# Optimization experiments

Hardware: AMD Instinct MI355X
Metric: run time of the kernel (lower is better)

The kernel has to match this reference:

```python
import jax, jax.numpy as jnp
import numpy as np

NUM_EXPERTS = 8
TOP_K = 2
IN_DIM = 2048
BOT_DIM = 512
BATCH, SEQ = 4, 2048


def setup_inputs() -> dict:
    key = jax.random.key(0)
    ks = jax.random.split(key, 8)
    scale_d = 1.0 / np.sqrt(IN_DIM)
    scale_b = 1.0 / np.sqrt(BOT_DIM)
    return {
        "hidden_states": jax.random.normal(ks[0], (BATCH, SEQ, IN_DIM), jnp.float32),
        # gate: nn.Linear(in_dim, num_experts, bias=False) -> weight [E, D]
        "gate_w": jax.random.normal(ks[1], (NUM_EXPERTS, IN_DIM), jnp.float32) * scale_d,
        # routed experts: down weight [E, B, D], down bias [E, B], up weight [E, D, B], up bias [E, D]
        # (original inits up weights/biases to zero; use small random so grads are non-trivial)
        "wd": jax.random.normal(ks[2], (NUM_EXPERTS, BOT_DIM, IN_DIM), jnp.float32) * scale_d,
        "bd": jnp.zeros((NUM_EXPERTS, BOT_DIM), jnp.float32),
        "wu": jax.random.normal(ks[3], (NUM_EXPERTS, IN_DIM, BOT_DIM), jnp.float32) * scale_b * 0.02,
        "bu": jnp.zeros((NUM_EXPERTS, IN_DIM), jnp.float32),
        # one shared Bottleneck_adapter
        "ws_d": jax.random.normal(ks[4], (BOT_DIM, IN_DIM), jnp.float32) * scale_d,
        "bs_d": jnp.zeros((BOT_DIM,), jnp.float32),
        "ws_u": jax.random.normal(ks[5], (IN_DIM, BOT_DIM), jnp.float32) * scale_b * 0.02,
        "bs_u": jnp.zeros((IN_DIM,), jnp.float32),
    }


def _gelu(x):
    # torch.nn.GELU() default = exact erf form
    return jax.nn.gelu(x, approximate=False)


def reference(hidden_states, gate_w, wd, bd, wu, bu, ws_d, bs_d, ws_u, bs_u):
    B, S, D = hidden_states.shape
    x = hidden_states.reshape(-1, D)                      # [T, D]
    T = x.shape[0]

    # --- top-k softmax routing (softmax in fp32, renormalize top-k weights) ---
    logits = x @ gate_w.T                                 # [T, E]
    probs = jax.nn.softmax(logits.astype(jnp.float32), axis=-1)
    rw, sel = jax.lax.top_k(probs, TOP_K)                 # [T, K]
    rw = rw / rw.sum(axis=-1, keepdims=True)
    rw = rw.astype(x.dtype)

    # dense combine weights [T, E]: zero for unselected experts == skipping them
    combine = jnp.zeros((T, NUM_EXPERTS), x.dtype).at[
        jnp.arange(T)[:, None], sel
    ].add(rw)

    # --- routed experts: bottleneck FFN per expert, combined by routing weight ---
    down = jnp.einsum('td,ebd->teb', x, wd) + bd[None]    # [T, E, Bn]
    h = _gelu(down) * combine[:, :, None]                 # weight before up-proj (linear)
    expert_out = jnp.einsum('teb,edb->td', h, wu) + combine @ bu  # [T, D]

    # --- shared expert (applied to original hidden states) ---
    shared = _gelu(x @ ws_d.T + bs_d) @ ws_u.T + bs_u

    out = (expert_out + shared).reshape(B, S, D)
    return out
```

## Files before the change

kernel.cpp:

```cpp
#include <hip/hip_runtime.h>
#include <hip/hip_bf16.h>

typedef __bf16 bf16_t;
typedef __bf16 bf16x8 __attribute__((ext_vector_type(8)));
typedef float f32x4 __attribute__((ext_vector_type(4)));

#define T_TOK 8192
#define D_IN  2048
#define D_BOT 512
#define MAXTILES 192
#define MAXDTILES 200

union U4B8 { uint4 u; bf16x8 b; };
__device__ __forceinline__ bf16x8 as_bf16x8(uint4 u) { U4B8 x; x.u = u; return x.b; }
__device__ __forceinline__ uint4 as_uint4(bf16x8 b) { U4B8 x; x.b = b; return x.u; }

typedef const __attribute__((address_space(1))) void gas_void;
typedef __attribute__((address_space(3))) void las_void;
__device__ __forceinline__ void async16(const void* g, void* l) {
    __builtin_amdgcn_global_load_lds((gas_void*)g, (las_void*)l, 16, 0, 0);
}

__device__ __forceinline__ uint4 ld_cvt8(const float* __restrict__ p) {
    f32x4 a0 = ((const f32x4*)p)[0];
    f32x4 a1 = ((const f32x4*)p)[1];
    bf16x8 v;
    v[0] = (bf16_t)a0[0]; v[1] = (bf16_t)a0[1]; v[2] = (bf16_t)a0[2]; v[3] = (bf16_t)a0[3];
    v[4] = (bf16_t)a1[0]; v[5] = (bf16_t)a1[1]; v[6] = (bf16_t)a1[2]; v[7] = (bf16_t)a1[3];
    return as_uint4(v);
}

__device__ __forceinline__ float gelu_f(float v) {
    return 0.5f * v * (1.0f + erff(v * 0.7071067811865476f));
}

__global__ __launch_bounds__(256) void cvt_kernel(const float* __restrict__ src,
                                                  bf16_t* __restrict__ dst, int n8) {
    const int i = blockIdx.x * 256 + threadIdx.x;
    if (i < n8) ((uint4*)dst)[i] = ld_cvt8(src + (size_t)i * 8);
}

__global__ __launch_bounds__(256) void cvt4_kernel(const float* __restrict__ wd,
                                                   const float* __restrict__ wsd,
                                                   const float* __restrict__ wu,
                                                   const float* __restrict__ wsu,
                                                   bf16_t* __restrict__ WallD,
                                                   bf16_t* __restrict__ WallU) {
    const int i = blockIdx.x * 256 + threadIdx.x;
    const int N0 = 4096 * 2048 / 8;
    const int N1 = N0 + 512 * 2048 / 8;
    const int N2 = N1 + 8 * 2048 * 512 / 8;
    const int N3 = N2 + 2048 * 512 / 8;
    if (i < N0)      ((uint4*)WallD)[i] = ld_cvt8(wd + (size_t)i * 8);
    else if (i < N1) ((uint4*)WallD)[i] = ld_cvt8(wsd + (size_t)(i - N0) * 8);
    else if (i < N2) ((uint4*)WallU)[i - N1] = ld_cvt8(wu + (size_t)(i - N1) * 8);
    else if (i < N3) ((uint4*)WallU)[i - N1] = ld_cvt8(wsu + (size_t)(i - N2) * 8);
}

__global__ __launch_bounds__(256) void gate_kernel(const float* __restrict__ x,
                                                   const float* __restrict__ gw,
                                                   float* __restrict__ combine,
                                                   int* __restrict__ sel,
                                                   bf16_t* __restrict__ Xbf) {
    const int wave = threadIdx.x >> 6, lane = threadIdx.x & 63;
    const int t = blockIdx.x * 4 + wave;
    const float* xrow = x + (size_t)t * D_IN;
    f32x4 xa[4][2];
#pragma unroll
    for (int c = 0; c < 4; ++c) {
        const float* p = xrow + c * 512 + lane * 8;
        xa[c][0] = ((const f32x4*)p)[0];
        xa[c][1] = ((const f32x4*)p)[1];
    }
#pragma unroll
    for (int c = 0; c < 4; ++c) {
        bf16x8 v;
#pragma unroll
        for (int j = 0; j < 4; ++j) { v[j] = (bf16_t)xa[c][0][j]; v[4 + j] = (bf16_t)xa[c][1][j]; }
        *(uint4*)(Xbf + (size_t)t * D_IN + c * 512 + lane * 8) = as_uint4(v);
    }
    float p[8];
#pragma unroll
    for (int e = 0; e < 8; ++e) {
        const float* gr = gw + e * D_IN;
        float s = 0.f;
#pragma unroll
        for (int c = 0; c < 4; ++c) {
            const float* q = gr + c * 512 + lane * 8;
            f32x4 g0 = ((const f32x4*)q)[0], g1 = ((const f32x4*)q)[1];
#pragma unroll
            for (int j = 0; j < 4; ++j) s += xa[c][0][j] * g0[j] + xa[c][1][j] * g1[j];
        }
#pragma unroll
        for (int off = 32; off > 0; off >>= 1) s += __shfl_xor(s, off, 64);
        p[e] = s;
    }
    float m = p[0];
#pragma unroll
    for (int e = 1; e < 8; ++e) m = fmaxf(m, p[e]);
    float sum = 0.f;
#pragma unroll
    for (int e = 0; e < 8; ++e) { p[e] = expf(p[e] - m); sum += p[e]; }
    const float inv = 1.0f / sum;
#pragma unroll
    for (int e = 0; e < 8; ++e) p[e] *= inv;
    int i0 = 0;
#pragma unroll
    for (int e = 1; e < 8; ++e) if (p[e] > p[i0]) i0 = e;
    int i1 = -1;
#pragma unroll
    for (int e = 0; e < 8; ++e) { if (e == i0) continue; if (i1 < 0 || p[e] > p[i1]) i1 = e; }
    const float rs = 1.0f / (p[i0] + p[i1]);
    if (lane < 8)
        combine[t * 8 + lane] = (lane == i0) ? p[i0] * rs : (lane == i1) ? p[i1] * rs : 0.0f;
    if (lane == 0) sel[t] = i0 | (i1 << 4);
}

__global__ __launch_bounds__(256) void build_kernel(const int* __restrict__ sel,
                                                    int* __restrict__ meta,
                                                    int* __restrict__ tokE,
                                                    int* __restrict__ tokP) {
    __shared__ unsigned short cAll[8][256];
    __shared__ unsigned short cP[64][256];
    const int tid = threadIdx.x;
#pragma unroll
    for (int e = 0; e < 8; ++e) cAll[e][tid] = 0;
#pragma unroll
    for (int p = 0; p < 64; ++p) cP[p][tid] = 0;
    __syncthreads();
    int sl[32];
#pragma unroll
    for (int j = 0; j < 32; ++j) sl[j] = sel[tid * 32 + j];
#pragma unroll
    for (int j = 0; j < 32; ++j) {
        const int e0 = sl[j] & 15, e1 = sl[j] >> 4;
        cAll[e0][tid]++; cAll[e1][tid]++; cP[e0 * 8 + e1][tid]++;
    }
    __syncthreads();
    if (tid < 8) {
        unsigned short* arr = cAll[tid];
        int run = 0;
        for (int i = 0; i < 256; ++i) { int v = arr[i]; arr[i] = (unsigned short)run; run += v; }
        meta[tid] = run;
    } else if (tid >= 64 && tid < 128) {
        unsigned short* arr = cP[tid - 64];
        int run = 0;
        for (int i = 0; i < 256; ++i) { int v = arr[i]; arr[i] = (unsigned short)run; run += v; }
        meta[64 + (tid - 64)] = run;
    }
    __syncthreads();
    if (tid == 0) {
        int nt = 0;
        for (int p = 0; p < 64; ++p) {
            const int c = meta[64 + p];
            for (int s = 0; s < c; s += 64) { meta[128 + nt] = p; meta[320 + nt] = s; ++nt; }
        }
        meta[8] = nt;
        int nd = 0;
        for (int e = 0; e < 9; ++e) {
            const int c = (e < 8) ? meta[e] : T_TOK;
            for (int s = 0; s < c; s += 128) { meta[512 + nd] = e; meta[768 + nd] = s; ++nd; }
        }
        meta[9] = nd;
    }
#pragma unroll
    for (int j = 0; j < 32; ++j) {
        const int t = tid * 32 + j, e0 = sl[j] & 15, e1 = sl[j] >> 4;
        const int p0 = cAll[e0][tid]++;  tokE[e0 * 8192 + p0] = t;
        const int p1 = cAll[e1][tid]++;  tokE[e1 * 8192 + p1] = t | 65536;
        const int q  = cP[e0 * 8 + e1][tid]++;  tokP[(e0 * 8 + e1) * 8192 + q] = t;
    }
}

__global__ __launch_bounds__(256) void down_kernel(const bf16_t* __restrict__ Xbf,
                                                   const bf16_t* __restrict__ Wall,
                                                   const float* __restrict__ Bd,
                                                   const float* __restrict__ Bsd,
                                                   const float* __restrict__ combine,
                                                   const int* __restrict__ meta,
                                                   const int* __restrict__ tokE,
                                                   bf16_t* __restrict__ Ht) {
    __shared__ uint4 As4[128 * 8];
    __shared__ uint4 Bs4[64 * 8];
    const int orig = blockIdx.x;
    const int swz = (orig & 7) * 200 + (orig >> 3);
    const int yt = swz >> 3;
    const int tile_n = (swz & 7) * 64;
    if (yt >= meta[9]) return;
    const int e = meta[512 + yt];
    const int m0 = meta[768 + yt];
    const int count = (e < 8) ? meta[e] : T_TOK;
    const int tid = threadIdx.x, lane = tid & 63, wv = tid >> 6;
    const int wm = wv >> 1, wn = wv & 1;
    const int gB = (lane & 7) ^ ((lane >> 3) & 7);

    const bf16_t* aAddr[4];
    const bf16_t* bAddr[2];
#pragma unroll
    for (int j = 0; j < 4; ++j) {
        const int rr = (wv * 4 + j) * 8 + (lane >> 3);
        int gi = m0 + rr; if (gi > count - 1) gi = count - 1;
        const int t = (e < 8) ? (tokE[e * 8192 + gi] & 0xFFFF) : gi;
        aAddr[j] = Xbf + (size_t)t * D_IN + gB * 8;
    }
#pragma unroll
    for (int j = 0; j < 2; ++j) {
        const int rr = (wv * 2 + j) * 8 + (lane >> 3);
        bAddr[j] = Wall + (size_t)(e * 512 + tile_n + rr) * D_IN + gB * 8;
    }

    f32x4 acc[4][2];
#pragma unroll
    for (int i = 0; i < 4; ++i)
#pragma unroll
        for (int j = 0; j < 2; ++j) acc[i][j] = (f32x4){0.f, 0.f, 0.f, 0.f};

    for (int kt = 0; kt < D_IN / 64; ++kt) {
        const int k0 = kt * 64;
#pragma unroll
        for (int j = 0; j < 4; ++j)
            async16(aAddr[j] + k0, &As4[(wv * 4 + j) * 64]);
#pragma unroll
        for (int j = 0; j < 2; ++j)
            async16(bAddr[j] + k0, &Bs4[(wv * 2 + j) * 64]);
        __syncthreads();
#pragma unroll
        for (int ks = 0; ks < 2; ++ks) {
            bf16x8 af[4], bfr[2];
#pragma unroll
            for (int i = 0; i < 4; ++i) {
                const int ar = wm * 64 + i * 16 + (lane & 15);
                af[i] = as_bf16x8(As4[ar * 8 + ((ks * 4 + (lane >> 4)) ^ (lane & 7))]);
            }
#pragma unroll
            for (int i = 0; i < 2; ++i) {
                const int br = wn * 32 + i * 16 + (lane & 15);
                bfr[i] = as_bf16x8(Bs4[br * 8 + ((ks * 4 + (lane >> 4)) ^ (lane & 7))]);
            }
#pragma unroll
            for (int mi = 0; mi < 4; ++mi)
#pragma unroll
                for (int nj = 0; nj < 2; ++nj)
                    acc[mi][nj] = __builtin_amdgcn_mfma_f32_16x16x32_bf16(
                        af[mi], bfr[nj], acc[mi][nj], 0, 0, 0);
        }
        __syncthreads();
    }

#pragma unroll
    for (int nj = 0; nj < 2; ++nj) {
        const int nn = tile_n + wn * 32 + nj * 16 + (lane & 15);
        const float bias = (e < 8) ? Bd[e * 512 + nn] : Bsd[nn];
#pragma unroll
        for (int mi = 0; mi < 4; ++mi) {
            const int g0 = m0 + wm * 64 + mi * 16 + ((lane >> 4) << 2);
#pragma unroll
            for (int r = 0; r < 4; ++r) {
                const int gi = g0 + r;
                if (gi >= count) continue;
                if (e < 8) {
                    const int entry = tokE[e * 8192 + gi];
                    const int t = entry & 0xFFFF, rank = entry >> 16;
                    const float v = gelu_f(acc[mi][nj][r] + bias) * combine[t * 8 + e];
                    Ht[(size_t)t * 1536 + rank * 512 + nn] = (bf16_t)v;
                } else {
                    Ht[(size_t)gi * 1536 + 1024 + nn] = (bf16_t)gelu_f(acc[mi][nj][r] + bias);
                }
            }
        }
    }
}

__global__ __launch_bounds__(256) void up_kernel(const bf16_t* __restrict__ Ht,
                                                 const bf16_t* __restrict__ Wup,
                                                 const float* __restrict__ Bu,
                                                 const float* __restrict__ Bsu,
                                                 const float* __restrict__ combine,
                                                 const int* __restrict__ meta,
                                                 const int* __restrict__ tokP,
                                                 float* __restrict__ Out) {
    __shared__ uint4 As4[64 * 8];
    __shared__ uint4 Bs4[128 * 8];
    const int orig = blockIdx.x;
    const int swz = (orig & 7) * 384 + (orig >> 3);
    const int yt = swz >> 4;
    const int tile_n = (swz & 15) * 128;
    if (yt >= meta[8]) return;
    const int p = meta[128 + yt], s = meta[320 + yt];
    const int e0 = p >> 3, e1 = p & 7;
    const int cntP = meta[64 + p];
    const int tid = threadIdx.x, lane = tid & 63, wv = tid >> 6;
    const int wm = wv >> 1, wn = wv & 1;
    const int gB = (lane & 7) ^ ((lane >> 3) & 7);

    const bf16_t* aAddr[2];
#pragma unroll
    for (int j = 0; j < 2; ++j) {
        const int rr = (wv * 2 + j) * 8 + (lane >> 3);
        int gi = s + rr; if (gi > cntP - 1) gi = cntP - 1;
        const int t = tokP[p * 8192 + gi];
        aAddr[j] = Ht + (size_t)t * 1536 + gB * 8;
    }
    size_t bRow[4];
#pragma unroll
    for (int j = 0; j < 4; ++j) {
        const int rr = (wv * 4 + j) * 8 + (lane >> 3);
        bRow[j] = (size_t)(tile_n + rr) * D_BOT + gB * 8;
    }

    f32x4 acc[2][4];
#pragma unroll
    for (int i = 0; i < 2; ++i)
#pragma unroll
        for (int j = 0; j < 4; ++j) acc[i][j] = (f32x4){0.f, 0.f, 0.f, 0.f};

    for (int kt = 0; kt < 24; ++kt) {
        const int seg = kt >> 3;
        const int slot = (seg == 0) ? e0 : (seg == 1) ? e1 : 8;
        const bf16_t* wbase = Wup + (size_t)slot * (D_IN * D_BOT) + (kt & 7) * 64;
#pragma unroll
        for (int j = 0; j < 2; ++j)
            async16(aAddr[j] + kt * 64, &As4[(wv * 2 + j) * 64]);
#pragma unroll
        for (int j = 0; j < 4; ++j)
            async16(wbase + bRow[j], &Bs4[(wv * 4 + j) * 64]);
        __syncthreads();
#pragma unroll
        for (int ks = 0; ks < 2; ++ks) {
            bf16x8 af[2], bfr[4];
#pragma unroll
            for (int i = 0; i < 2; ++i) {
                const int ar = wm * 32 + i * 16 + (lane & 15);
                af[i] = as_bf16x8(As4[ar * 8 + ((ks * 4 + (lane >> 4)) ^ (lane & 7))]);
            }
#pragma unroll
            for (int i = 0; i < 4; ++i) {
                const int br = wn * 64 + i * 16 + (lane & 15);
                bfr[i] = as_bf16x8(Bs4[br * 8 + ((ks * 4 + (lane >> 4)) ^ (lane & 7))]);
            }
#pragma unroll
            for (int mi = 0; mi < 2; ++mi)
#pragma unroll
                for (int nj = 0; nj < 4; ++nj)
                    acc[mi][nj] = __builtin_amdgcn_mfma_f32_16x16x32_bf16(
                        af[mi], bfr[nj], acc[mi][nj], 0, 0, 0);
        }
        __syncthreads();
    }

#pragma unroll
    for (int nj = 0; nj < 4; ++nj) {
        const int d = tile_n + wn * 64 + nj * 16 + (lane & 15);
        const float bu0 = Bu[e0 * D_IN + d], bu1 = Bu[e1 * D_IN + d], bs = Bsu[d];
#pragma unroll
        for (int mi = 0; mi < 2; ++mi) {
            const int r0 = wm * 32 + mi * 16 + ((lane >> 4) << 2);
#pragma unroll
            for (int r = 0; r < 4; ++r) {
                const int gi = s + r0 + r;
                if (gi >= cntP) continue;
                const int t = tokP[p * 8192 + gi];
                const float c0 = combine[t * 8 + e0], c1 = combine[t * 8 + e1];
                Out[(size_t)t * D_IN + d] = acc[mi][nj][r] + c0 * bu0 + c1 * bu1 + bs;
            }
        }
    }
}

extern "C" void kernel_launch(void* const* d_in, const int* in_sizes, int n_in,
                              void* d_out, int out_size, void* d_ws, size_t ws_size,
                              hipStream_t stream) {
    const float* x   = (const float*)d_in[0];
    const float* gw  = (const float*)d_in[1];
    const float* wd  = (const float*)d_in[2];
    const float* bd  = (const float*)d_in[3];
    const float* wu  = (const float*)d_in[4];
    const float* bu  = (const float*)d_in[5];
    const float* wsd = (const float*)d_in[6];
    const float* bsd = (const float*)d_in[7];
    const float* wsu = (const float*)d_in[8];
    const float* bsu = (const float*)d_in[9];
    float* out = (float*)d_out;

    char* ws = (char*)d_ws;
    float* combine = (float*)(ws + 0);
    int*   meta    = (int*)(ws + 262144);
    int*   sel     = (int*)(ws + 266240);
    int*   tokE    = (int*)(ws + 299008);
    int*   tokP    = (int*)(ws + 561152);
    bf16_t* Xbf    = (bf16_t*)(ws + 2658304);
    bf16_t* Ht     = (bf16_t*)(ws + 36212736ull);
    bf16_t* WallD  = (bf16_t*)(ws + 61378560ull);
    const size_t NEED_SEP = 61378560ull + 2ull * 18874368ull;
    const bool separate = (ws_size >= NEED_SEP);
    bf16_t* WallU  = separate ? (bf16_t*)(ws + 61378560ull + 18874368ull) : WallD;

    gate_kernel<<<T_TOK / 4, 256, 0, stream>>>(x, gw, combine, sel, Xbf);
    build_kernel<<<1, 256, 0, stream>>>(sel, meta, tokE, tokP);

    if (separate) {
        cvt4_kernel<<<9216, 256, 0, stream>>>(wd, wsd, wu, wsu, WallD, WallU);
        down_kernel<<<MAXDTILES * 8, 256, 0, stream>>>(Xbf, WallD, bd, bsd, combine, meta, tokE, Ht);
        up_kernel<<<MAXTILES * 16, 256, 0, stream>>>(Ht, WallU, bu, bsu, combine, meta, tokP, out);
    } else {
        cvt_kernel<<<(4096 * D_IN / 8) / 256, 256, 0, stream>>>(wd, WallD, 4096 * D_IN / 8);
        cvt_kernel<<<(512 * D_IN / 8) / 256, 256, 0, stream>>>(wsd, WallD + (size_t)4096 * D_IN, 512 * D_IN / 8);
        down_kernel<<<MAXDTILES * 8, 256, 0, stream>>>(Xbf, WallD, bd, bsd, combine, meta, tokE, Ht);
        cvt_kernel<<<(8 * D_IN * D_BOT / 8) / 256, 256, 0, stream>>>(wu, WallD, 8 * D_IN * D_BOT / 8);
        cvt_kernel<<<(D_IN * D_BOT / 8) / 256, 256, 0, stream>>>(wsu, WallD + (size_t)8 * D_IN * D_BOT, D_IN * D_BOT / 8);
        up_kernel<<<MAXTILES * 16, 256, 0, stream>>>(Ht, WallD, bu, bsu, combine, meta, tokP, out);
    }
}
```

Before: 450.9 us.

## Double-buffer LDS tiles in down and up GEMM kernels with async prefetch

Both grouped GEMM kernels now keep two LDS buffers and issue global-to-LDS async loads two k-steps ahead, waiting with explicit vmcnt counters before each compute step. The aim is to hide global memory latency behind MFMA work, where previously every k-step loaded and then stalled on a full sync. This doubles LDS use per block, which may lower occupancy, and it depends on manual waitcnt values matching the count of outstanding loads (6 per stage).

```diff
diff --git a/kernel.cpp b/kernel.cpp
--- a/kernel.cpp
+++ b/kernel.cpp
@@ -180,8 +180,8 @@
                                                    const int* __restrict__ meta,
                                                    const int* __restrict__ tokE,
                                                    bf16_t* __restrict__ Ht) {
-    __shared__ uint4 As4[128 * 8];
-    __shared__ uint4 Bs4[64 * 8];
+    __shared__ uint4 As4[2][128 * 8];
+    __shared__ uint4 Bs4[2][64 * 8];
     const int orig = blockIdx.x;
     const int swz = (orig & 7) * 200 + (orig >> 3);
     const int yt = swz >> 3;
@@ -215,27 +215,28 @@
 #pragma unroll
         for (int j = 0; j < 2; ++j) acc[i][j] = (f32x4){0.f, 0.f, 0.f, 0.f};
 
-    for (int kt = 0; kt < D_IN / 64; ++kt) {
+    auto stage = [&](int b, int kt) {
         const int k0 = kt * 64;
 #pragma unroll
         for (int j = 0; j < 4; ++j)
-            async16(aAddr[j] + k0, &As4[(wv * 4 + j) * 64]);
+            async16(aAddr[j] + k0, &As4[b][(wv * 4 + j) * 64]);
 #pragma unroll
         for (int j = 0; j < 2; ++j)
-            async16(bAddr[j] + k0, &Bs4[(wv * 2 + j) * 64]);
-        __syncthreads();
+            async16(bAddr[j] + k0, &Bs4[b][(wv * 2 + j) * 64]);
+    };
+    auto compute = [&](int b) {
 #pragma unroll
         for (int ks = 0; ks < 2; ++ks) {
             bf16x8 af[4], bfr[2];
 #pragma unroll
             for (int i = 0; i < 4; ++i) {
                 const int ar = wm * 64 + i * 16 + (lane & 15);
-                af[i] = as_bf16x8(As4[ar * 8 + ((ks * 4 + (lane >> 4)) ^ (lane & 7))]);
+                af[i] = as_bf16x8(As4[b][ar * 8 + ((ks * 4 + (lane >> 4)) ^ (lane & 7))]);
             }
 #pragma unroll
             for (int i = 0; i < 2; ++i) {
                 const int br = wn * 32 + i * 16 + (lane & 15);
-                bfr[i] = as_bf16x8(Bs4[br * 8 + ((ks * 4 + (lane >> 4)) ^ (lane & 7))]);
+                bfr[i] = as_bf16x8(Bs4[b][br * 8 + ((ks * 4 + (lane >> 4)) ^ (lane & 7))]);
             }
 #pragma unroll
             for (int mi = 0; mi < 4; ++mi)
@@ -244,7 +245,18 @@
                     acc[mi][nj] = __builtin_amdgcn_mfma_f32_16x16x32_bf16(
                         af[mi], bfr[nj], acc[mi][nj], 0, 0, 0);
         }
-        __syncthreads();
+    };
+
+    const int NT = D_IN / 64;
+    stage(0, 0);
+    stage(1, 1);
+    for (int kt = 0; kt < NT; ++kt) {
+        if (kt == NT - 1) asm volatile("s_waitcnt vmcnt(0)" ::: "memory");
+        else              asm volatile("s_waitcnt vmcnt(6)" ::: "memory");
+        __builtin_amdgcn_s_barrier();
+        compute(kt & 1);
+        __builtin_amdgcn_s_barrier();
+        if (kt + 2 < NT) stage(kt & 1, kt + 2);
     }
 
 #pragma unroll
@@ -279,8 +291,8 @@
                                                  const int* __restrict__ meta,
                                                  const int* __restrict__ tokP,
                                                  float* __restrict__ Out) {
-    __shared__ uint4 As4[64 * 8];
-    __shared__ uint4 Bs4[128 * 8];
+    __shared__ uint4 As4[2][64 * 8];
+    __shared__ uint4 Bs4[2][128 * 8];
     const int orig = blockIdx.x;
     const int swz = (orig & 7) * 384 + (orig >> 3);
     const int yt = swz >> 4;
@@ -314,29 +326,30 @@
 #pragma unroll
         for (int j = 0; j < 4; ++j) acc[i][j] = (f32x4){0.f, 0.f, 0.f, 0.f};
 
-    for (int kt = 0; kt < 24; ++kt) {
+    auto stage = [&](int b, int kt) {
         const int seg = kt >> 3;
         const int slot = (seg == 0) ? e0 : (seg == 1) ? e1 : 8;
         const bf16_t* wbase = Wup + (size_t)slot * (D_IN * D_BOT) + (kt & 7) * 64;
 #pragma unroll
         for (int j = 0; j < 2; ++j)
-            async16(aAddr[j] + kt * 64, &As4[(wv * 2 + j) * 64]);
+            async16(aAddr[j] + kt * 64, &As4[b][(wv * 2 + j) * 64]);
 #pragma unroll
         for (int j = 0; j < 4; ++j)
-            async16(wbase + bRow[j], &Bs4[(wv * 4 + j) * 64]);
-        __syncthreads();
+            async16(wbase + bRow[j], &Bs4[b][(wv * 4 + j) * 64]);
+    };
+    auto compute = [&](int b) {
 #pragma unroll
         for (int ks = 0; ks < 2; ++ks) {
             bf16x8 af[2], bfr[4];
 #pragma unroll
             for (int i = 0; i < 2; ++i) {
                 const int ar = wm * 32 + i * 16 + (lane & 15);
-                af[i] = as_bf16x8(As4[ar * 8 + ((ks * 4 + (lane >> 4)) ^ (lane & 7))]);
+                af[i] = as_bf16x8(As4[b][ar * 8 + ((ks * 4 + (lane >> 4)) ^ (lane & 7))]);
             }
 #pragma unroll
             for (int i = 0; i < 4; ++i) {
                 const int br = wn * 64 + i * 16 + (lane & 15);
-                bfr[i] = as_bf16x8(Bs4[br * 8 + ((ks * 4 + (lane >> 4)) ^ (lane & 7))]);
+                bfr[i] = as_bf16x8(Bs4[b][br * 8 + ((ks * 4 + (lane >> 4)) ^ (lane & 7))]);
             }
 #pragma unroll
             for (int mi = 0; mi < 2; ++mi)
@@ -345,7 +358,18 @@
                     acc[mi][nj] = __builtin_amdgcn_mfma_f32_16x16x32_bf16(
                         af[mi], bfr[nj], acc[mi][nj], 0, 0, 0);
         }
-        __syncthreads();
+    };
+
+    const int NT = 24;
+    stage(0, 0);
+    stage(1, 1);
+    for (int kt = 0; kt < NT; ++kt) {
+        if (kt == NT - 1) asm volatile("s_waitcnt vmcnt(0)" ::: "memory");
+        else              asm volatile("s_waitcnt vmcnt(6)" ::: "memory");
+        __builtin_amdgcn_s_barrier();
+        compute(kt & 1);
+        __builtin_amdgcn_s_barrier();
+        if (kt + 2 < NT) stage(kt & 1, kt + 2);
     }
 
 #pragma unroll
```

After: 496.1 us. +10.0%, slower.

## Merge gate with weight conversion and run GEMM kernels with 512-thread blocks

Applied to the files above, without the earlier changes.

Combines the gating/routing kernel and the fp32-to-bf16 weight conversion into one launch so the two independent jobs share the GPU and one launch is saved. The down and up GEMM kernels move to 8 waves per block, each wave holding a smaller accumulator tile (2x2 MFMA fragments) and issuing fewer async loads. This aims to raise occupancy and latency hiding, but more waves contend on the per-k-step barrier, and the block tile shapes appear unchanged.

```diff
diff --git a/kernel.cpp b/kernel.cpp
--- a/kernel.cpp
+++ b/kernel.cpp
@@ -40,13 +40,87 @@
     if (i < n8) ((uint4*)dst)[i] = ld_cvt8(src + (size_t)i * 8);
 }
 
-__global__ __launch_bounds__(256) void cvt4_kernel(const float* __restrict__ wd,
-                                                   const float* __restrict__ wsd,
-                                                   const float* __restrict__ wu,
-                                                   const float* __restrict__ wsu,
-                                                   bf16_t* __restrict__ WallD,
-                                                   bf16_t* __restrict__ WallU) {
-    const int i = blockIdx.x * 256 + threadIdx.x;
+__device__ __forceinline__ void gate_body(int bid,
+                                          const float* __restrict__ x,
+                                          const float* __restrict__ gw,
+                                          float* __restrict__ combine,
+                                          int* __restrict__ sel,
+                                          bf16_t* __restrict__ Xbf) {
+    const int wave = threadIdx.x >> 6, lane = threadIdx.x & 63;
+    const int t = bid * 4 + wave;
+    const float* xrow = x + (size_t)t * D_IN;
+    f32x4 xa[4][2];
+#pragma unroll
+    for (int c = 0; c < 4; ++c) {
+        const float* p = xrow + c * 512 + lane * 8;
+        xa[c][0] = ((const f32x4*)p)[0];
+        xa[c][1] = ((const f32x4*)p)[1];
+    }
+#pragma unroll
+    for (int c = 0; c < 4; ++c) {
+        bf16x8 v;
+#pragma unroll
+        for (int j = 0; j < 4; ++j) { v[j] = (bf16_t)xa[c][0][j]; v[4 + j] = (bf16_t)xa[c][1][j]; }
+        *(uint4*)(Xbf + (size_t)t * D_IN + c * 512 + lane * 8) = as_uint4(v);
+    }
+    float p[8];
+#pragma unroll
+    for (int e = 0; e < 8; ++e) {
+        const float* gr = gw + e * D_IN;
+        float s = 0.f;
+#pragma unroll
+        for (int c = 0; c < 4; ++c) {
+            const float* q = gr + c * 512 + lane * 8;
+            f32x4 g0 = ((const f32x4*)q)[0], g1 = ((const f32x4*)q)[1];
+#pragma unroll
+            for (int j = 0; j < 4; ++j) s += xa[c][0][j] * g0[j] + xa[c][1][j] * g1[j];
+        }
+#pragma unroll
+        for (int off = 32; off > 0; off >>= 1) s += __shfl_xor(s, off, 64);
+        p[e] = s;
+    }
+    float m = p[0];
+#pragma unroll
+    for (int e = 1; e < 8; ++e) m = fmaxf(m, p[e]);
+    float sum = 0.f;
+#pragma unroll
+    for (int e = 0; e < 8; ++e) { p[e] = expf(p[e] - m); sum += p[e]; }
+    const float inv = 1.0f / sum;
+#pragma unroll
+    for (int e = 0; e < 8; ++e) p[e] *= inv;
+    int i0 = 0;
+#pragma unroll
+    for (int e = 1; e < 8; ++e) if (p[e] > p[i0]) i0 = e;
+    int i1 = -1;
+#pragma unroll
+    for (int e = 0; e < 8; ++e) { if (e == i0) continue; if (i1 < 0 || p[e] > p[i1]) i1 = e; }
+    const float rs = 1.0f / (p[i0] + p[i1]);
+    if (lane < 8)
+        combine[t * 8 + lane] = (lane == i0) ? p[i0] * rs : (lane == i1) ? p[i1] * rs : 0.0f;
+    if (lane == 0) sel[t] = i0 | (i1 << 4);
+}
+
+__global__ __launch_bounds__(256) void gate_kernel(const float* __restrict__ x,
+                                                   const float* __restrict__ gw,
+                                                   float* __restrict__ combine,
+                                                   int* __restrict__ sel,
+                                                   bf16_t* __restrict__ Xbf) {
+    gate_body(blockIdx.x, x, gw, combine, sel, Xbf);
+}
+
+__global__ __launch_bounds__(256) void gate_cvt_kernel(const float* __restrict__ x,
+                                                       const float* __restrict__ gw,
+                                                       float* __restrict__ combine,
+                                                       int* __restrict__ sel,
+                                                       bf16_t* __restrict__ Xbf,
+                                                       const float* __restrict__ wd,
+                                                       const float* __restrict__ wsd,
+                                                       const float* __restrict__ wu,
+                                                       const float* __restrict__ wsu,
+                                                       bf16_t* __restrict__ WallD,
+                                                       bf16_t* __restrict__ WallU) {
+    if (blockIdx.x < 2048) { gate_body(blockIdx.x, x, gw, combine, sel, Xbf); return; }
+    const int i = (blockIdx.x - 2048) * 256 + threadIdx.x;
     const int N0 = 4096 * 2048 / 8;
     const int N1 = N0 + 512 * 2048 / 8;
     const int N2 = N1 + 8 * 2048 * 512 / 8;
@@ -55,65 +129,6 @@
     else if (i < N1) ((uint4*)WallD)[i] = ld_cvt8(wsd + (size_t)(i - N0) * 8);
     else if (i < N2) ((uint4*)WallU)[i - N1] = ld_cvt8(wu + (size_t)(i - N1) * 8);
     else if (i < N3) ((uint4*)WallU)[i - N1] = ld_cvt8(wsu + (size_t)(i - N2) * 8);
-}
-
-__global__ __launch_bounds__(256) void gate_kernel(const float* __restrict__ x,
-                                                   const float* __restrict__ gw,
-                                                   float* __restrict__ combine,
-                                                   int* __restrict__ sel,
-                                                   bf16_t* __restrict__ Xbf) {
-    const int wave = threadIdx.x >> 6, lane = threadIdx.x & 63;
-    const int t = blockIdx.x * 4 + wave;
-    const float* xrow = x + (size_t)t * D_IN;
-    f32x4 xa[4][2];
-#pragma unroll
-    for (int c = 0; c < 4; ++c) {
-        const float* p = xrow + c * 512 + lane * 8;
-        xa[c][0] = ((const f32x4*)p)[0];
-        xa[c][1] = ((const f32x4*)p)[1];
-    }
-#pragma unroll
-    for (int c = 0; c < 4; ++c) {
-        bf16x8 v;
-#pragma unroll
-        for (int j = 0; j < 4; ++j) { v[j] = (bf16_t)xa[c][0][j]; v[4 + j] = (bf16_t)xa[c][1][j]; }
-        *(uint4*)(Xbf + (size_t)t * D_IN + c * 512 + lane * 8) = as_uint4(v);
-    }
-    float p[8];
-#pragma unroll
-    for (int e = 0; e < 8; ++e) {
-        const float* gr = gw + e * D_IN;
-        float s = 0.f;
-#pragma unroll
-        for (int c = 0; c < 4; ++c) {
-            const float* q = gr + c * 512 + lane * 8;
-            f32x4 g0 = ((const f32x4*)q)[0], g1 = ((const f32x4*)q)[1];
-#pragma unroll
-            for (int j = 0; j < 4; ++j) s += xa[c][0][j] * g0[j] + xa[c][1][j] * g1[j];
-        }
-#pragma unroll
-        for (int off = 32; off > 0; off >>= 1) s += __shfl_xor(s, off, 64);
-        p[e] = s;
-    }
-    float m = p[0];
-#pragma unroll
-    for (int e = 1; e < 8; ++e) m = fmaxf(m, p[e]);
-    float sum = 0.f;
-#pragma unroll
-    for (int e = 0; e < 8; ++e) { p[e] = expf(p[e] - m); sum += p[e]; }
-    const float inv = 1.0f / sum;
-#pragma unroll
-    for (int e = 0; e < 8; ++e) p[e] *= inv;
-    int i0 = 0;
-#pragma unroll
-    for (int e = 1; e < 8; ++e) if (p[e] > p[i0]) i0 = e;
-    int i1 = -1;
-#pragma unroll
-    for (int e = 0; e < 8; ++e) { if (e == i0) continue; if (i1 < 0 || p[e] > p[i1]) i1 = e; }
-    const float rs = 1.0f / (p[i0] + p[i1]);
-    if (lane < 8)
-        combine[t * 8 + lane] = (lane == i0) ? p[i0] * rs : (lane == i1) ? p[i1] * rs : 0.0f;
-    if (lane == 0) sel[t] = i0 | (i1 << 4);
 }
 
 __global__ __launch_bounds__(256) void build_kernel(const int* __restrict__ sel,
@@ -172,7 +187,7 @@
     }
 }
 
-__global__ __launch_bounds__(256) void down_kernel(const bf16_t* __restrict__ Xbf,
+__global__ __launch_bounds__(512) void down_kernel(const bf16_t* __restrict__ Xbf,
                                                    const bf16_t* __restrict__ Wall,
                                                    const float* __restrict__ Bd,
                                                    const float* __restrict__ Bsd,
@@ -194,42 +209,39 @@
     const int wm = wv >> 1, wn = wv & 1;
     const int gB = (lane & 7) ^ ((lane >> 3) & 7);
 
-    const bf16_t* aAddr[4];
-    const bf16_t* bAddr[2];
-#pragma unroll
-    for (int j = 0; j < 4; ++j) {
-        const int rr = (wv * 4 + j) * 8 + (lane >> 3);
+    const bf16_t* aAddr[2];
+#pragma unroll
+    for (int j = 0; j < 2; ++j) {
+        const int rr = (wv * 2 + j) * 8 + (lane >> 3);
         int gi = m0 + rr; if (gi > count - 1) gi = count - 1;
         const int t = (e < 8) ? (tokE[e * 8192 + gi] & 0xFFFF) : gi;
         aAddr[j] = Xbf + (size_t)t * D_IN + gB * 8;
     }
-#pragma unroll
-    for (int j = 0; j < 2; ++j) {
-        const int rr = (wv * 2 + j) * 8 + (lane >> 3);
-        bAddr[j] = Wall + (size_t)(e * 512 + tile_n + rr) * D_IN + gB * 8;
-    }
-
-    f32x4 acc[4][2];
-#pragma unroll
-    for (int i = 0; i < 4; ++i)
+    const bf16_t* bAddr;
+    {
+        const int rr = wv * 8 + (lane >> 3);
+        bAddr = Wall + (size_t)(e * 512 + tile_n + rr) * D_IN + gB * 8;
+    }
+
+    f32x4 acc[2][2];
+#pragma unroll
+    for (int i = 0; i < 2; ++i)
 #pragma unroll
         for (int j = 0; j < 2; ++j) acc[i][j] = (f32x4){0.f, 0.f, 0.f, 0.f};
 
     for (int kt = 0; kt < D_IN / 64; ++kt) {
         const int k0 = kt * 64;
 #pragma unroll
-        for (int j = 0; j < 4; ++j)
-            async16(aAddr[j] + k0, &As4[(wv * 4 + j) * 64]);
-#pragma unroll
         for (int j = 0; j < 2; ++j)
-            async16(bAddr[j] + k0, &Bs4[(wv * 2 + j) * 64]);
+            async16(aAddr[j] + k0, &As4[(wv * 2 + j) * 64]);
+        async16(bAddr + k0, &Bs4[wv * 64]);
         __syncthreads();
 #pragma unroll
         for (int ks = 0; ks < 2; ++ks) {
-            bf16x8 af[4], bfr[2];
-#pragma unroll
-            for (int i = 0; i < 4; ++i) {
-                const int ar = wm * 64 + i * 16 + (lane & 15);
+            bf16x8 af[2], bfr[2];
+#pragma unroll
+            for (int i = 0; i < 2; ++i) {
+                const int ar = wm * 32 + i * 16 + (lane & 15);
                 af[i] = as_bf16x8(As4[ar * 8 + ((ks * 4 + (lane >> 4)) ^ (lane & 7))]);
             }
 #pragma unroll
@@ -238,7 +250,7 @@
                 bfr[i] = as_bf16x8(Bs4[br * 8 + ((ks * 4 + (lane >> 4)) ^ (lane & 7))]);
             }
 #pragma unroll
-            for (int mi = 0; mi < 4; ++mi)
+            for (int mi = 0; mi < 2; ++mi)
 #pragma unroll
                 for (int nj = 0; nj < 2; ++nj)
                     acc[mi][nj] = __builtin_amdgcn_mfma_f32_16x16x32_bf16(
@@ -252,8 +264,8 @@
         const int nn = tile_n + wn * 32 + nj * 16 + (lane & 15);
         const float bias = (e < 8) ? Bd[e * 512 + nn] : Bsd[nn];
 #pragma unroll
-        for (int mi = 0; mi < 4; ++mi) {
-            const int g0 = m0 + wm * 64 + mi * 16 + ((lane >> 4) << 2);
+        for (int mi = 0; mi < 2; ++mi) {
+            const int g0 = m0 + wm * 32 + mi * 16 + ((lane >> 4) << 2);
 #pragma unroll
             for (int r = 0; r < 4; ++r) {
                 const int gi = g0 + r;
@@ -271,7 +283,7 @@
     }
 }
 
-__global__ __launch_bounds__(256) void up_kernel(const bf16_t* __restrict__ Ht,
+__global__ __launch_bounds__(512) void up_kernel(const bf16_t* __restrict__ Ht,
                                                  const bf16_t* __restrict__ Wup,
                                                  const float* __restrict__ Bu,
                                                  const float* __restrict__ Bsu,
@@ -290,58 +302,55 @@
     const int e0 = p >> 3, e1 = p & 7;
     const int cntP = meta[64 + p];
     const int tid = threadIdx.x, lane = tid & 63, wv = tid >> 6;
-    const int wm = wv >> 1, wn = wv & 1;
+    const int wm = wv >> 2, wn = wv & 3;
     const int gB = (lane & 7) ^ ((lane >> 3) & 7);
 
-    const bf16_t* aAddr[2];
+    const bf16_t* aAddr;
+    {
+        const int rr = wv * 8 + (lane >> 3);
+        int gi = s + rr; if (gi > cntP - 1) gi = cntP - 1;
+        const int t = tokP[p * 8192 + gi];
+        aAddr = Ht + (size_t)t * 1536 + gB * 8;
+    }
+    size_t bRow[2];
 #pragma unroll
     for (int j = 0; j < 2; ++j) {
         const int rr = (wv * 2 + j) * 8 + (lane >> 3);
-        int gi = s + rr; if (gi > cntP - 1) gi = cntP - 1;
-        const int t = tokP[p * 8192 + gi];
-        aAddr[j] = Ht + (size_t)t * 1536 + gB * 8;
-    }
-    size_t bRow[4];
-#pragma unroll
-    for (int j = 0; j < 4; ++j) {
-        const int rr = (wv * 4 + j) * 8 + (lane >> 3);
         bRow[j] = (size_t)(tile_n + rr) * D_BOT + gB * 8;
     }
 
-    f32x4 acc[2][4];
+    f32x4 acc[2][2];
 #pragma unroll
     for (int i = 0; i < 2; ++i)
 #pragma unroll
-        for (int j = 0; j < 4; ++j) acc[i][j] = (f32x4){0.f, 0.f, 0.f, 0.f};
+        for (int j = 0; j < 2; ++j) acc[i][j] = (f32x4){0.f, 0.f, 0.f, 0.f};
 
     for (int kt = 0; kt < 24; ++kt) {
         const int seg = kt >> 3;
         const int slot = (seg == 0) ? e0 : (seg == 1) ? e1 : 8;
         const bf16_t* wbase = Wup + (size_t)slot * (D_IN * D_BOT) + (kt & 7) * 64;
+        async16(aAddr + kt * 64, &As4[wv * 64]);
 #pragma unroll
         for (int j = 0; j < 2; ++j)
-            async16(aAddr[j] + kt * 64, &As4[(wv * 2 + j) * 64]);
-#pragma unroll
-        for (int j = 0; j < 4; ++j)
-            async16(wbase + bRow[j], &Bs4[(wv * 4 + j) * 64]);
+            async16(wbase + bRow[j], &Bs4[(wv * 2 + j) * 64]);
         __syncthreads();
 #pragma unroll
         for (int ks = 0; ks < 2; ++ks) {
-            bf16x8 af[2], bfr[4];
+            bf16x8 af[2], bfr[2];
 #pragma unroll
             for (int i = 0; i < 2; ++i) {
                 const int ar = wm * 32 + i * 16 + (lane & 15);
                 af[i] = as_bf16x8(As4[ar * 8 + ((ks * 4 + (lane >> 4)) ^ (lane & 7))]);
             }
 #pragma unroll
-            for (int i = 0; i < 4; ++i) {
-                const int br = wn * 64 + i * 16 + (lane & 15);
+            for (int i = 0; i < 2; ++i) {
+                const int br = wn * 32 + i * 16 + (lane & 15);
                 bfr[i] = as_bf16x8(Bs4[br * 8 + ((ks * 4 + (lane >> 4)) ^ (lane & 7))]);
             }
 #pragma unroll
             for (int mi = 0; mi < 2; ++mi)
 #pragma unroll
-                for (int nj = 0; nj < 4; ++nj)
+                for (int nj = 0; nj < 2; ++nj)
                     acc[mi][nj] = __builtin_amdgcn_mfma_f32_16x16x32_bf16(
                         af[mi], bfr[nj], acc[mi][nj], 0, 0, 0);
         }
@@ -349,8 +358,8 @@
     }
 
 #pragma unroll
-    for (int nj = 0; nj < 4; ++nj) {
-        const int d = tile_n + wn * 64 + nj * 16 + (lane & 15);
+    for (int nj = 0; nj < 2; ++nj) {
+        const int d = tile_n + wn * 32 + nj * 16 + (lane & 15);
         const float bu0 = Bu[e0 * D_IN + d], bu1 = Bu[e1 * D_IN + d], bs = Bsu[d];
 #pragma unroll
         for (int mi = 0; mi < 2; ++mi) {
@@ -395,19 +404,20 @@
     const bool separate = (ws_size >= NEED_SEP);
     bf16_t* WallU  = separate ? (bf16_t*)(ws + 61378560ull + 18874368ull) : WallD;
 
-    gate_kernel<<<T_TOK / 4, 256, 0, stream>>>(x, gw, combine, sel, Xbf);
-    build_kernel<<<1, 256, 0, stream>>>(sel, meta, tokE, tokP);
-
     if (separate) {
-        cvt4_kernel<<<9216, 256, 0, stream>>>(wd, wsd, wu, wsu, WallD, WallU);
-        down_kernel<<<MAXDTILES * 8, 256, 0, stream>>>(Xbf, WallD, bd, bsd, combine, meta, tokE, Ht);
-        up_kernel<<<MAXTILES * 16, 256, 0, stream>>>(Ht, WallU, bu, bsu, combine, meta, tokP, out);
+        gate_cvt_kernel<<<2048 + 9216, 256, 0, stream>>>(x, gw, combine, sel, Xbf,
+                                                         wd, wsd, wu, wsu, WallD, WallU);
+        build_kernel<<<1, 256, 0, stream>>>(sel, meta, tokE, tokP);
+        down_kernel<<<MAXDTILES * 8, 512, 0, stream>>>(Xbf, WallD, bd, bsd, combine, meta, tokE, Ht);
+        up_kernel<<<MAXTILES * 16, 512, 0, stream>>>(Ht, WallU, bu, bsu, combine, meta, tokP, out);
     } else {
+        gate_kernel<<<T_TOK / 4, 256, 0, stream>>>(x, gw, combine, sel, Xbf);
+        build_kernel<<<1, 256, 0, stream>>>(sel, meta, tokE, tokP);
         cvt_kernel<<<(4096 * D_IN / 8) / 256, 256, 0, stream>>>(wd, WallD, 4096 * D_IN / 8);
         cvt_kernel<<<(512 * D_IN / 8) / 256, 256, 0, stream>>>(wsd, WallD + (size_t)4096 * D_IN, 512 * D_IN / 8);
-        down_kernel<<<MAXDTILES * 8, 256, 0, stream>>>(Xbf, WallD, bd, bsd, combine, meta, tokE, Ht);
+        down_kernel<<<MAXDTILES * 8, 512, 0, stream>>>(Xbf, WallD, bd, bsd, combine, meta, tokE, Ht);
         cvt_kernel<<<(8 * D_IN * D_BOT / 8) / 256, 256, 0, stream>>>(wu, WallD, 8 * D_IN * D_BOT / 8);
         cvt_kernel<<<(D_IN * D_BOT / 8) / 256, 256, 0, stream>>>(wsu, WallD + (size_t)8 * D_IN * D_BOT, D_IN * D_BOT / 8);
-        up_kernel<<<MAXTILES * 16, 256, 0, stream>>>(Ht, WallD, bu, bsu, combine, meta, tokP, out);
-    }
-}
+        up_kernel<<<MAXTILES * 16, 512, 0, stream>>>(Ht, WallD, bu, bsu, combine, meta, tokP, out);
+    }
+}
```

Measured after the change: 428.6 us, median of 2. 1.05x faster.
